# Kernel optimization log

Hardware: AMD Instinct MI355X
Metric: run time of the kernel (lower is better)

The kernel has to match this reference:

```python
import jax, jax.numpy as jnp
import numpy as np

N_EMBD = 2048
N_HEAD = 16
N_KV_HEAD = 4
HEAD_DIM = N_EMBD // N_HEAD
MAX_SEQ_LEN = 2048
EPS = 1e-6
ROPE_THETA = 10000.0


def _build_rope_cache(dim, max_seq_len, theta=ROPE_THETA):
    inv_freq = 1.0 / theta ** (np.arange(0, dim, 2, dtype=np.float32) / dim)
    t = np.arange(max_seq_len, dtype=np.float32)
    freqs = np.outer(t, inv_freq)
    emb = np.concatenate([freqs, freqs], axis=-1)
    return jnp.asarray(np.cos(emb)), jnp.asarray(np.sin(emb))


def _rotate_half(x):
    x1, x2 = jnp.split(x, 2, axis=-1)
    return jnp.concatenate([-x2, x1], axis=-1)


def _rms_norm(x, w, eps=EPS):
    var = jnp.mean(jnp.square(x), axis=-1, keepdims=True)
    return x * jax.lax.rsqrt(var + eps) * w


def setup_inputs() -> dict:
    key = jax.random.key(0)
    ks = jax.random.split(key, 7)
    s = 1.0 / np.sqrt(N_EMBD)
    kv_dim = N_KV_HEAD * HEAD_DIM
    x = jax.random.normal(ks[0], (2, 2048, N_EMBD), dtype=jnp.float32)
    Wq = jax.random.normal(ks[1], (N_EMBD, N_EMBD), dtype=jnp.float32) * s
    Wk = jax.random.normal(ks[2], (kv_dim, N_EMBD), dtype=jnp.float32) * s
    Wv = jax.random.normal(ks[3], (kv_dim, N_EMBD), dtype=jnp.float32) * s
    Wo = jax.random.normal(ks[4], (N_EMBD, N_EMBD), dtype=jnp.float32) * s
    qn_w = jnp.ones((HEAD_DIM,), dtype=jnp.float32)
    kn_w = jnp.ones((HEAD_DIM,), dtype=jnp.float32)
    cos, sin = _build_rope_cache(HEAD_DIM, MAX_SEQ_LEN)
    return {"x": x, "Wq": Wq, "Wk": Wk, "Wv": Wv, "Wo": Wo,
            "qn_w": qn_w, "kn_w": kn_w, "rope_cos": cos, "rope_sin": sin}


def reference(x, Wq, Wk, Wv, Wo, qn_w, kn_w, rope_cos, rope_sin):
    B, T, C = x.shape
    # projections (torch Linear: y = x @ W.T)
    q = jnp.einsum('btc,dc->btd', x, Wq).reshape(B, T, N_HEAD, HEAD_DIM).transpose(0, 2, 1, 3)
    k = jnp.einsum('btc,dc->btd', x, Wk).reshape(B, T, N_KV_HEAD, HEAD_DIM).transpose(0, 2, 1, 3)
    v = jnp.einsum('btc,dc->btd', x, Wv).reshape(B, T, N_KV_HEAD, HEAD_DIM).transpose(0, 2, 1, 3)
    # qk rms-norm
    q = _rms_norm(q, qn_w)
    k = _rms_norm(k, kn_w)
    # rope
    cos = rope_cos[:T][None, None]  # [1,1,T,D]
    sin = rope_sin[:T][None, None]
    q = q * cos + _rotate_half(q) * sin
    k = k * cos + _rotate_half(k) * sin
    # GQA broadcast: group queries over kv heads instead of repeating k/v
    G = N_HEAD // N_KV_HEAD
    qg = q.reshape(B, N_KV_HEAD, G, T, HEAD_DIM)
    scale = 1.0 / jnp.sqrt(jnp.asarray(HEAD_DIM, dtype=q.dtype))
    scores = jnp.einsum('bhgqd,bhkd->bhgqk', qg, k) * scale  # [B,KV,G,T,T]
    causal = jnp.tril(jnp.ones((T, T), dtype=bool))
    scores = jnp.where(causal, scores, jnp.asarray(-jnp.inf, dtype=scores.dtype))
    attn = jax.nn.softmax(scores, axis=-1)
    y = jnp.einsum('bhgqk,bhkd->bhgqd', attn, v)  # [B,KV,G,T,D]
    y = y.reshape(B, N_HEAD, T, HEAD_DIM).transpose(0, 2, 1, 3).reshape(B, T, C)
    return jnp.einsum('btc,dc->btd', y, Wo)
```

## Files before the change

kernel.cpp:

```cpp
#include <hip/hip_runtime.h>
#include <stdint.h>

typedef unsigned short u16;
typedef __attribute__((ext_vector_type(4))) float f32x4;
typedef __attribute__((ext_vector_type(16))) float f32x16;
typedef __attribute__((ext_vector_type(8))) short bf16x8;
typedef __attribute__((ext_vector_type(4))) unsigned short u16x4;
typedef __attribute__((ext_vector_type(4))) unsigned u32x4;

static __device__ __forceinline__ u16 f2bf(float f) {
  union { float f; unsigned u; } v; v.f = f;
  unsigned r = v.u + 0x7fffu + ((v.u >> 16) & 1u);
  return (u16)(r >> 16);
}

static __device__ __forceinline__ unsigned cvtpk(float lo, float hi) {
  unsigned r;
  asm("v_cvt_pk_bf16_f32 %0, %1, %2" : "=v"(r) : "v"(lo), "v"(hi));
  return r;
}

static __device__ __forceinline__ void plane32_swap(unsigned& a, unsigned& b) {
  asm volatile("v_permlane32_swap_b32 %0, %1" : "+v"(a), "+v"(b));
}

static __device__ __forceinline__ float exp2_fast(float x) {
  float r;
  asm("v_exp_f32 %0, %1" : "=v"(r) : "v"(x));
  return r;
}

static __device__ __forceinline__ void load_lds16(const void* g, void* l) {
  __builtin_amdgcn_global_load_lds(
      (const __attribute__((address_space(1))) void*)g,
      (__attribute__((address_space(3))) void*)l, 16, 0, 0);
}


__global__ __launch_bounds__(256) void cvt_f32_bf16(
    const float* __restrict__ in, u16* __restrict__ out, int n) {
  int i = blockIdx.x * 256 + threadIdx.x;
  const int n4 = n >> 2;
  for (; i < n4; i += gridDim.x * 256) {
    f32x4 v = *(const f32x4*)(in + (size_t)i * 4);
    u16x4 o = { f2bf(v[0]), f2bf(v[1]), f2bf(v[2]), f2bf(v[3]) };
    *(u16x4*)(out + (size_t)i * 4) = o;
  }
}

__global__ __launch_bounds__(256) void build_wcat(
    const float* __restrict__ Wq, const float* __restrict__ Wk,
    const float* __restrict__ Wv, u16* __restrict__ out) {
  int i = blockIdx.x * 256 + threadIdx.x;
  const int n4 = 3072 * 512;
  for (; i < n4; i += gridDim.x * 256) {
    int row = i >> 9;
    int c4 = i & 511;
    const float* src;
    if (row < 2048)       src = Wq + (size_t)row * 2048;
    else if (row < 2560)  src = Wk + (size_t)(row - 2048) * 2048;
    else                  src = Wv + (size_t)(row - 2560) * 2048;
    f32x4 v = *(const f32x4*)(src + c4 * 4);
    u16x4 o = { f2bf(v[0]), f2bf(v[1]), f2bf(v[2]), f2bf(v[3]) };
    *(u16x4*)(out + (size_t)i * 4) = o;
  }
}

__global__ __launch_bounds__(256) void gemm_bt(
    const u16* __restrict__ A, const u16* __restrict__ B,
    float* __restrict__ C, int M, int N, int K) {
  __shared__ u16 As[128 * 32];
  __shared__ u16 Bs[128 * 32];
  const int tid = threadIdx.x;
  const int lin = blockIdx.x;
  const int x = lin & 7, t = lin >> 3;
  const int bm = x * 4 + (t & 3);
  const int bn = t >> 2;
  const int w = tid >> 6, l = tid & 63;
  const int wr = w >> 1, wc = w & 1;
  const int lr = l & 15, lg = l >> 4;
  f32x4 acc[4][4] = {};
  const int srow = tid >> 2;
  const int scol = (tid & 3) << 3;
  const u16* Ag = A + (size_t)bm * 128 * K + (size_t)srow * K + scol;
  const u16* Bg = B + (size_t)bn * 128 * K + (size_t)srow * K + scol;
  u16* Asl = As + srow * 32 + scol;
  u16* Bsl = Bs + srow * 32 + scol;
  const int nk = K >> 5;
  for (int kt = 0; kt < nk; ++kt) {
    __syncthreads();
    const int ko = kt << 5;
    load_lds16(Ag + ko, Asl);
    load_lds16(Ag + (size_t)64 * K + ko, Asl + 64 * 32);
    load_lds16(Bg + ko, Bsl);
    load_lds16(Bg + (size_t)64 * K + ko, Bsl + 64 * 32);
    __syncthreads();
    bf16x8 af[4], bfr[4];
#pragma unroll
    for (int m = 0; m < 4; ++m)
      af[m] = *(const bf16x8*)&As[(wr * 64 + m * 16 + lr) * 32 + lg * 8];
#pragma unroll
    for (int n = 0; n < 4; ++n)
      bfr[n] = *(const bf16x8*)&Bs[(wc * 64 + n * 16 + lr) * 32 + lg * 8];
#pragma unroll
    for (int m = 0; m < 4; ++m)
#pragma unroll
      for (int n = 0; n < 4; ++n)
        acc[m][n] = __builtin_amdgcn_mfma_f32_16x16x32_bf16(af[m], bfr[n], acc[m][n], 0, 0, 0);
  }
#pragma unroll
  for (int m = 0; m < 4; ++m) {
    const int row = bm * 128 + wr * 64 + m * 16 + lg * 4;
#pragma unroll
    for (int n = 0; n < 4; ++n) {
      const int col = bn * 128 + wc * 64 + n * 16 + lr;
#pragma unroll
      for (int r = 0; r < 4; ++r)
        C[(size_t)(row + r) * N + col] = acc[m][n][r];
    }
  }
}

__global__ __launch_bounds__(256) void norm_rope(
    const float* __restrict__ qkv, const float* __restrict__ qn_w,
    const float* __restrict__ kn_w, const float* __restrict__ cosb,
    const float* __restrict__ sinb, u16* __restrict__ qhat,
    u16* __restrict__ khat) {
  const int gw = (blockIdx.x * 256 + threadIdx.x) >> 6;
  const int lane = threadIdx.x & 63;
  const int slot = gw % 20;
  const int row = gw / 20;
  const int t = row & 2047;
  const int b = row >> 11;
  const float* src; const float* nw; u16* dst;
  bool isq = slot < 16;
  if (isq) {
    src = qkv + (size_t)row * 3072 + slot * 128;
    nw = qn_w;
    dst = qhat + ((size_t)(b * 16 + slot) * 2048 + t) * 128;
  } else {
    src = qkv + (size_t)row * 3072 + 2048 + (slot - 16) * 128;
    nw = kn_w;
    dst = khat + ((size_t)(b * 4 + (slot - 16)) * 2048 + t) * 128;
  }
  float x1 = src[lane], x2 = src[lane + 64];
  float ss = x1 * x1 + x2 * x2;
#pragma unroll
  for (int o = 32; o; o >>= 1) ss += __shfl_xor(ss, o);
  float rs = rsqrtf(ss * (1.0f / 128.0f) + 1e-6f);
  float h1 = x1 * rs * nw[lane];
  float h2 = x2 * rs * nw[lane + 64];
  float c = cosb[t * 128 + lane], s = sinb[t * 128 + lane];
  float o1 = h1 * c - h2 * s;
  float o2 = h2 * c + h1 * s;
  if (isq) { o1 *= 0.12751744752f; o2 *= 0.12751744752f; }
  dst[lane] = f2bf(o1);
  dst[lane + 64] = f2bf(o2);
}

__global__ __launch_bounds__(256) void v_trans(
    const float* __restrict__ qkv, u16* __restrict__ vT) {
  __shared__ u16 st[64][130];
  const int bi = blockIdx.x;
  const int tt = bi & 31;
  const int kv = (bi >> 5) & 3;
  const int b = bi >> 7;
  const int tid = threadIdx.x;
#pragma unroll
  for (int i = 0; i < 32; ++i) {
    int idx = i * 256 + tid;
    int t = idx >> 7, d = idx & 127;
    float v = qkv[(size_t)(b * 2048 + tt * 64 + t) * 3072 + 2560 + kv * 128 + d];
    st[t][d] = f2bf(v);
  }
  __syncthreads();
#pragma unroll
  for (int i = 0; i < 32; ++i) {
    int idx = i * 256 + tid;
    int d = idx >> 6, t = idx & 63;
    vT[((size_t)(b * 4 + kv) * 128 + d) * 2048 + tt * 64 + t] = st[t][d];
  }
}

__global__ __launch_bounds__(512, 2) void attn(
    const u16* __restrict__ qhat, const u16* __restrict__ khat,
    const u16* __restrict__ vT, u16* __restrict__ yb) {
  __shared__ u16 Kt[2][64 * 128];
  __shared__ u16 Vt[2][128 * 64];
  const int bi = blockIdx.x;
  const int s = bi & 7;
  const int bh = bi >> 3;
  const int h = bh & 15, b = bh >> 4;
  const int kvh = h >> 2;
  const int tid = threadIdx.x;
  const int w = tid >> 6, l = tid & 63;
  const int ws = w & 3;
  const int cw = (w < 4) ? s : (15 - s);
  const int ql = l & 31, hi = l >> 5;
  const int wq0 = cw * 128 + ws * 32;
  const int wq_end = wq0 + 31;
  const int qg = wq0 + ql;

  bf16x8 qf[8];
  const u16* qp = qhat + ((size_t)(b * 16 + h) * 2048 + qg) * 128 + hi * 8;
#pragma unroll
  for (int sf = 0; sf < 8; ++sf) qf[sf] = *(const bf16x8*)(qp + 16 * sf);

  f32x16 yacc[4] = {};
  float m = -1e30f, lsum = 0.f;

  const u16* Kg = khat + (size_t)(b * 4 + kvh) * 2048 * 128;
  const u16* Vg = vT + (size_t)(b * 4 + kvh) * 128 * 2048;
  const int nt = 32 - 2 * s;

  auto stageK = [&](int tile, int buf) {
#pragma unroll
    for (int j = 0; j < 2; ++j) {
      int idx = j * 512 + tid;
      int row = idx >> 4, ch = idx & 15;
      load_lds16(Kg + (size_t)(tile * 64 + row) * 128 + ((ch ^ (row & 7)) * 8),
                 &Kt[buf][idx * 8]);
    }
  };
  auto stageV = [&](int tile, int buf) {
#pragma unroll
    for (int j = 0; j < 2; ++j) {
      int idx = j * 512 + tid;
      int row = idx >> 3, ch = idx & 7;
      load_lds16(Vg + (size_t)row * 2048 + tile * 64 + ((ch ^ (row & 7)) * 8),
                 &Vt[buf][idx * 8]);
    }
  };

  stageK(0, 0);
  stageV(0, 0);
  int cur = 0;
  for (int tile = 0; tile < nt; ++tile) {
    const int kv0 = tile * 64;
    __syncthreads();
    if (tile + 1 < nt) { stageK(tile + 1, cur ^ 1); stageV(tile + 1, cur ^ 1); }
    if (kv0 <= wq_end) {
      const u16* Kc = Kt[cur];
      const u16* Vc = Vt[cur];
      f32x16 sacc[2] = {};
      __builtin_amdgcn_s_setprio(1);
#pragma unroll
      for (int n = 0; n < 2; ++n) {
#pragma unroll
        for (int sf = 0; sf < 8; ++sf) {
          bf16x8 kf = *(const bf16x8*)&Kc[(n * 32 + ql) * 128 + (((2 * sf + hi) ^ (l & 7)) * 8)];
          sacc[n] = __builtin_amdgcn_mfma_f32_32x32x16_bf16(kf, qf[sf], sacc[n], 0, 0, 0);
        }
      }
      __builtin_amdgcn_s_setprio(0);
      if (kv0 + 63 > wq0) {
#pragma unroll
        for (int n = 0; n < 2; ++n)
#pragma unroll
          for (int r = 0; r < 16; ++r) {
            int kv = kv0 + n * 32 + (r & 3) + 8 * (r >> 2) + 4 * hi;
            if (kv > qg) sacc[n][r] = -1e30f;
          }
      }
      float pm = -1e30f;
#pragma unroll
      for (int n = 0; n < 2; ++n)
#pragma unroll
        for (int r = 0; r < 16; ++r) pm = fmaxf(pm, sacc[n][r]);
      pm = fmaxf(pm, __shfl_xor(pm, 32));
      if (!__all(pm - m <= 11.0f)) {
        float mn = fmaxf(m, pm);
        float sc = exp2_fast(m - mn);
        m = mn;
        lsum *= sc;
#pragma unroll
        for (int r = 0; r < 16; ++r) {
          int row = (r & 3) + 8 * (r >> 2) + 4 * hi;
          float scr = __shfl(sc, row);
#pragma unroll
          for (int d = 0; d < 4; ++d) yacc[d][r] *= scr;
        }
      }
      float ls = 0.f;
#pragma unroll
      for (int n = 0; n < 2; ++n)
#pragma unroll
        for (int r = 0; r < 16; ++r) {
          float e = exp2_fast(sacc[n][r] - m);
          sacc[n][r] = e;
          ls += e;
        }
      ls += __shfl_xor(ls, 32);
      lsum += ls;
      bf16x8 pa[4];
#pragma unroll
      for (int s4 = 0; s4 < 4; ++s4) {
        const int n = s4 >> 1, R = (s4 & 1) * 8;
        unsigned P01 = cvtpk(sacc[n][R + 0], sacc[n][R + 1]);
        unsigned P23 = cvtpk(sacc[n][R + 2], sacc[n][R + 3]);
        unsigned P45 = cvtpk(sacc[n][R + 4], sacc[n][R + 5]);
        unsigned P67 = cvtpk(sacc[n][R + 6], sacc[n][R + 7]);
        plane32_swap(P01, P45);
        plane32_swap(P23, P67);
        union { u32x4 u; bf16x8 bv; } cvu;
        cvu.u[0] = P01; cvu.u[1] = P23; cvu.u[2] = P45; cvu.u[3] = P67;
        pa[s4] = cvu.bv;
      }
      __builtin_amdgcn_s_setprio(1);
#pragma unroll
      for (int d = 0; d < 4; ++d) {
        const int rv = d * 32 + ql;
#pragma unroll
        for (int ks = 0; ks < 4; ++ks) {
          bf16x8 vf = *(const bf16x8*)&Vc[rv * 64 + (((ks * 2 + hi) ^ (rv & 7)) * 8)];
          yacc[d] = __builtin_amdgcn_mfma_f32_32x32x16_bf16(pa[ks], vf, yacc[d], 0, 0, 0);
        }
      }
      __builtin_amdgcn_s_setprio(0);
    }
    cur ^= 1;
  }
#pragma unroll
  for (int r = 0; r < 16; ++r) {
    int row = (r & 3) + 8 * (r >> 2) + 4 * hi;
    float li = __shfl(lsum, row);
    float inv = 1.0f / li;
    u16* yp = yb + ((size_t)(b * 2048) + wq0 + row) * 2048 + h * 128 + ql;
#pragma unroll
    for (int d = 0; d < 4; ++d) yp[d * 32] = f2bf(yacc[d][r] * inv);
  }
}


extern "C" void kernel_launch(void* const* d_in, const int* in_sizes, int n_in,
                              void* d_out, int out_size, void* d_ws, size_t ws_size,
                              hipStream_t stream) {
  const float* x    = (const float*)d_in[0];
  const float* Wq   = (const float*)d_in[1];
  const float* Wk   = (const float*)d_in[2];
  const float* Wv   = (const float*)d_in[3];
  const float* Wo   = (const float*)d_in[4];
  const float* qn   = (const float*)d_in[5];
  const float* kn   = (const float*)d_in[6];
  const float* cosb = (const float*)d_in[7];
  const float* sinb = (const float*)d_in[8];
  float* out = (float*)d_out;
  (void)in_sizes; (void)n_in; (void)out_size; (void)ws_size;

  char* p = (char*)d_ws;
  u16*   xb   = (u16*)p;   p += (size_t)8388608 * 2;
  u16*   wcat = (u16*)p;   p += (size_t)6291456 * 2;
  u16*   wob  = (u16*)p;   p += (size_t)4194304 * 2;
  float* qkvf = (float*)p; p += (size_t)12582912 * 4;
  u16*   qh   = (u16*)p;   p += (size_t)8388608 * 2;
  u16*   kh   = (u16*)p;   p += (size_t)2097152 * 2;
  u16*   vt   = (u16*)p;   p += (size_t)2097152 * 2;
  u16*   yb   = (u16*)p;   p += (size_t)8388608 * 2;

  cvt_f32_bf16<<<2048, 256, 0, stream>>>(x, xb, 8388608);
  build_wcat<<<2048, 256, 0, stream>>>(Wq, Wk, Wv, wcat);
  cvt_f32_bf16<<<2048, 256, 0, stream>>>(Wo, wob, 4194304);
  gemm_bt<<<768, 256, 0, stream>>>(xb, wcat, qkvf, 4096, 3072, 2048);
  norm_rope<<<20480, 256, 0, stream>>>(qkvf, qn, kn, cosb, sinb, qh, kh);
  v_trans<<<256, 256, 0, stream>>>(qkvf, vt);
  attn<<<256, 512, 0, stream>>>(qh, kh, vt, yb);
  gemm_bt<<<512, 256, 0, stream>>>(yb, wob, out, 4096, 2048, 2048);
}
```

Baseline: 242.1 us.

## Switch GEMM to 32x32x16 MFMA with XOR-swizzled LDS layout

Replaces the 16x16x32 bf16 MFMA tiling in gemm_bt with 32x32x16 MFMA tiles, using 2x2 f32x16 accumulators per wave. The global-to-LDS load now XOR-swizzles the 16-byte column chunk by row, so fragment reads from LDS avoid bank conflicts. This is meant to cut the number of LDS fragment loads and MFMA issues per K tile. The output write pattern changes to the 32x32 accumulator layout, and that store stays uncoalesced.

```diff
diff --git a/kernel.cpp b/kernel.cpp
--- a/kernel.cpp
+++ b/kernel.cpp
@@ -78,14 +78,14 @@
   const int bn = t >> 2;
   const int w = tid >> 6, l = tid & 63;
   const int wr = w >> 1, wc = w & 1;
-  const int lr = l & 15, lg = l >> 4;
-  f32x4 acc[4][4] = {};
+  const int ql = l & 31, hi = l >> 5;
+  f32x16 acc[2][2] = {};
   const int srow = tid >> 2;
-  const int scol = (tid & 3) << 3;
+  const int scol = (((tid & 3) ^ (srow & 3)) << 3);
   const u16* Ag = A + (size_t)bm * 128 * K + (size_t)srow * K + scol;
   const u16* Bg = B + (size_t)bn * 128 * K + (size_t)srow * K + scol;
-  u16* Asl = As + srow * 32 + scol;
-  u16* Bsl = Bs + srow * 32 + scol;
+  u16* Asl = As + tid * 8;
+  u16* Bsl = Bs + tid * 8;
   const int nk = K >> 5;
   for (int kt = 0; kt < nk; ++kt) {
     __syncthreads();
@@ -95,28 +95,36 @@
     load_lds16(Bg + ko, Bsl);
     load_lds16(Bg + (size_t)64 * K + ko, Bsl + 64 * 32);
     __syncthreads();
-    bf16x8 af[4], bfr[4];
-#pragma unroll
-    for (int m = 0; m < 4; ++m)
-      af[m] = *(const bf16x8*)&As[(wr * 64 + m * 16 + lr) * 32 + lg * 8];
-#pragma unroll
-    for (int n = 0; n < 4; ++n)
-      bfr[n] = *(const bf16x8*)&Bs[(wc * 64 + n * 16 + lr) * 32 + lg * 8];
-#pragma unroll
-    for (int m = 0; m < 4; ++m)
-#pragma unroll
-      for (int n = 0; n < 4; ++n)
-        acc[m][n] = __builtin_amdgcn_mfma_f32_16x16x32_bf16(af[m], bfr[n], acc[m][n], 0, 0, 0);
-  }
-#pragma unroll
-  for (int m = 0; m < 4; ++m) {
-    const int row = bm * 128 + wr * 64 + m * 16 + lg * 4;
-#pragma unroll
-    for (int n = 0; n < 4; ++n) {
-      const int col = bn * 128 + wc * 64 + n * 16 + lr;
-#pragma unroll
-      for (int r = 0; r < 4; ++r)
-        C[(size_t)(row + r) * N + col] = acc[m][n][r];
+#pragma unroll
+    for (int ks = 0; ks < 2; ++ks) {
+      const int e = ks * 2 + hi;
+      bf16x8 af[2], bfr[2];
+#pragma unroll
+      for (int ti = 0; ti < 2; ++ti) {
+        const int ra = wr * 64 + ti * 32 + ql;
+        const int rb = wc * 64 + ti * 32 + ql;
+        af[ti]  = *(const bf16x8*)&As[ra * 32 + ((e ^ (ra & 3)) << 3)];
+        bfr[ti] = *(const bf16x8*)&Bs[rb * 32 + ((e ^ (rb & 3)) << 3)];
+      }
+#pragma unroll
+      for (int mi = 0; mi < 2; ++mi)
+#pragma unroll
+        for (int ni = 0; ni < 2; ++ni)
+          acc[mi][ni] = __builtin_amdgcn_mfma_f32_32x32x16_bf16(
+              af[mi], bfr[ni], acc[mi][ni], 0, 0, 0);
+    }
+  }
+#pragma unroll
+  for (int mi = 0; mi < 2; ++mi) {
+    const int rb0 = bm * 128 + wr * 64 + mi * 32;
+#pragma unroll
+    for (int ni = 0; ni < 2; ++ni) {
+      const int col = bn * 128 + wc * 64 + ni * 32 + ql;
+#pragma unroll
+      for (int r = 0; r < 16; ++r) {
+        const int row = rb0 + (r & 3) + 8 * (r >> 2) + 4 * hi;
+        C[(size_t)row * N + col] = acc[mi][ni][r];
+      }
     }
   }
 }
```

New measurement: 238.2 us. No clear change (-1.6%).

## Rework GEMM to 32x32 MFMA with 64-deep swizzled LDS tiles and bf16 QKV output

Applied to the files above, without the earlier changes.

The GEMM core now uses 32x32x16 bf16 MFMA tiles with a K-step of 64, and the LDS layout is XOR-swizzled to avoid bank conflicts. This halves the number of barrier iterations and raises the math done per LDS read. The QKV projection now writes bf16 instead of fp32, which halves the intermediate traffic for norm_rope and v_trans. The cost is extra rounding of q/k before the RMS norm, and double the LDS per block.

```diff
diff --git a/kernel.cpp b/kernel.cpp
--- a/kernel.cpp
+++ b/kernel.cpp
@@ -12,6 +12,10 @@
   union { float f; unsigned u; } v; v.f = f;
   unsigned r = v.u + 0x7fffu + ((v.u >> 16) & 1u);
   return (u16)(r >> 16);
+}
+static __device__ __forceinline__ float bf2f(u16 u) {
+  union { unsigned u; float f; } v; v.u = ((unsigned)u) << 16;
+  return v.f;
 }
 
 static __device__ __forceinline__ unsigned cvtpk(float lo, float hi) {
@@ -66,63 +70,78 @@
   }
 }
 
+#define GEMM_CORE(C_STORE)                                                            \
+  __shared__ u16 As[128 * 64];                                                        \
+  __shared__ u16 Bs[128 * 64];                                                        \
+  const int tid = threadIdx.x;                                                        \
+  const int lin = blockIdx.x;                                                         \
+  const int x = lin & 7, t = lin >> 3;                              \
+  const int bm = x * 4 + (t & 3);                                                     \
+  const int bn = t >> 2;                                                              \
+  const int w = tid >> 6, l = tid & 63;                                               \
+  const int wr = w >> 1, wc = w & 1;                                                  \
+  const int ql = l & 31, hi = l >> 5;                                                 \
+  f32x16 acc[2][2] = {};                                                              \
+  const int nk = K >> 6;                                                              \
+  for (int kt = 0; kt < nk; ++kt) {                                                   \
+    __syncthreads();                                                                  \
+    const int ko = kt << 6;                                                           \
+    _Pragma("unroll")                                                                 \
+    for (int j = 0; j < 4; ++j) {                                                     \
+      int idx = j * 256 + tid;                                                        \
+      int row = idx >> 3, ch = idx & 7;                                               \
+      int col = ko + (((ch ^ (row & 7))) << 3);                                       \
+      load_lds16(A + (size_t)(bm * 128 + row) * K + col, As + idx * 8);               \
+      load_lds16(B + (size_t)(bn * 128 + row) * K + col, Bs + idx * 8);               \
+    }                                                                                 \
+    __syncthreads();                                                                  \
+    _Pragma("unroll")                                                                 \
+    for (int ks = 0; ks < 4; ++ks) {                                                  \
+      const int e = ks * 2 + hi;                                                      \
+      bf16x8 af[2], bfr[2];                                                           \
+      _Pragma("unroll")                                                               \
+      for (int ti = 0; ti < 2; ++ti) {                                                \
+        const int ra = wr * 64 + ti * 32 + ql;                                        \
+        const int rb = wc * 64 + ti * 32 + ql;                                        \
+        af[ti]  = *(const bf16x8*)&As[ra * 64 + ((e ^ (ra & 7)) << 3)];               \
+        bfr[ti] = *(const bf16x8*)&Bs[rb * 64 + ((e ^ (rb & 7)) << 3)];               \
+      }                                                                               \
+      _Pragma("unroll")                                                               \
+      for (int mi = 0; mi < 2; ++mi)                                                  \
+        _Pragma("unroll")                                                             \
+        for (int ni = 0; ni < 2; ++ni)                                                \
+          acc[mi][ni] = __builtin_amdgcn_mfma_f32_32x32x16_bf16(                      \
+              af[mi], bfr[ni], acc[mi][ni], 0, 0, 0);                                 \
+    }                                                                                 \
+  }                                                                                   \
+  _Pragma("unroll")                                                                   \
+  for (int mi = 0; mi < 2; ++mi) {                                                    \
+    const int rb0 = bm * 128 + wr * 64 + mi * 32;                                     \
+    _Pragma("unroll")                                                                 \
+    for (int ni = 0; ni < 2; ++ni) {                                                  \
+      const int col = bn * 128 + wc * 64 + ni * 32 + ql;                              \
+      _Pragma("unroll")                                                               \
+      for (int r = 0; r < 16; ++r) {                                                  \
+        const int row = rb0 + (r & 3) + 8 * (r >> 2) + 4 * hi;                        \
+        C_STORE;                                                                      \
+      }                                                                               \
+    }                                                                                 \
+  }
+
+__global__ __launch_bounds__(256) void gemm_bt16(
+    const u16* __restrict__ A, const u16* __restrict__ B,
+    u16* __restrict__ C, int M, int N, int K) {
+  GEMM_CORE(C[(size_t)row * N + col] = f2bf(acc[mi][ni][r]))
+}
+
 __global__ __launch_bounds__(256) void gemm_bt(
     const u16* __restrict__ A, const u16* __restrict__ B,
     float* __restrict__ C, int M, int N, int K) {
-  __shared__ u16 As[128 * 32];
-  __shared__ u16 Bs[128 * 32];
-  const int tid = threadIdx.x;
-  const int lin = blockIdx.x;
-  const int x = lin & 7, t = lin >> 3;
-  const int bm = x * 4 + (t & 3);
-  const int bn = t >> 2;
-  const int w = tid >> 6, l = tid & 63;
-  const int wr = w >> 1, wc = w & 1;
-  const int lr = l & 15, lg = l >> 4;
-  f32x4 acc[4][4] = {};
-  const int srow = tid >> 2;
-  const int scol = (tid & 3) << 3;
-  const u16* Ag = A + (size_t)bm * 128 * K + (size_t)srow * K + scol;
-  const u16* Bg = B + (size_t)bn * 128 * K + (size_t)srow * K + scol;
-  u16* Asl = As + srow * 32 + scol;
-  u16* Bsl = Bs + srow * 32 + scol;
-  const int nk = K >> 5;
-  for (int kt = 0; kt < nk; ++kt) {
-    __syncthreads();
-    const int ko = kt << 5;
-    load_lds16(Ag + ko, Asl);
-    load_lds16(Ag + (size_t)64 * K + ko, Asl + 64 * 32);
-    load_lds16(Bg + ko, Bsl);
-    load_lds16(Bg + (size_t)64 * K + ko, Bsl + 64 * 32);
-    __syncthreads();
-    bf16x8 af[4], bfr[4];
-#pragma unroll
-    for (int m = 0; m < 4; ++m)
-      af[m] = *(const bf16x8*)&As[(wr * 64 + m * 16 + lr) * 32 + lg * 8];
-#pragma unroll
-    for (int n = 0; n < 4; ++n)
-      bfr[n] = *(const bf16x8*)&Bs[(wc * 64 + n * 16 + lr) * 32 + lg * 8];
-#pragma unroll
-    for (int m = 0; m < 4; ++m)
-#pragma unroll
-      for (int n = 0; n < 4; ++n)
-        acc[m][n] = __builtin_amdgcn_mfma_f32_16x16x32_bf16(af[m], bfr[n], acc[m][n], 0, 0, 0);
-  }
-#pragma unroll
-  for (int m = 0; m < 4; ++m) {
-    const int row = bm * 128 + wr * 64 + m * 16 + lg * 4;
-#pragma unroll
-    for (int n = 0; n < 4; ++n) {
-      const int col = bn * 128 + wc * 64 + n * 16 + lr;
-#pragma unroll
-      for (int r = 0; r < 4; ++r)
-        C[(size_t)(row + r) * N + col] = acc[m][n][r];
-    }
-  }
+  GEMM_CORE(C[(size_t)row * N + col] = acc[mi][ni][r])
 }
 
 __global__ __launch_bounds__(256) void norm_rope(
-    const float* __restrict__ qkv, const float* __restrict__ qn_w,
+    const u16* __restrict__ qkv, const float* __restrict__ qn_w,
     const float* __restrict__ kn_w, const float* __restrict__ cosb,
     const float* __restrict__ sinb, u16* __restrict__ qhat,
     u16* __restrict__ khat) {
@@ -132,7 +151,7 @@
   const int row = gw / 20;
   const int t = row & 2047;
   const int b = row >> 11;
-  const float* src; const float* nw; u16* dst;
+  const u16* src; const float* nw; u16* dst;
   bool isq = slot < 16;
   if (isq) {
     src = qkv + (size_t)row * 3072 + slot * 128;
@@ -143,7 +162,7 @@
     nw = kn_w;
     dst = khat + ((size_t)(b * 4 + (slot - 16)) * 2048 + t) * 128;
   }
-  float x1 = src[lane], x2 = src[lane + 64];
+  float x1 = bf2f(src[lane]), x2 = bf2f(src[lane + 64]);
   float ss = x1 * x1 + x2 * x2;
 #pragma unroll
   for (int o = 32; o; o >>= 1) ss += __shfl_xor(ss, o);
@@ -159,7 +178,7 @@
 }
 
 __global__ __launch_bounds__(256) void v_trans(
-    const float* __restrict__ qkv, u16* __restrict__ vT) {
+    const u16* __restrict__ qkv, u16* __restrict__ vT) {
   __shared__ u16 st[64][130];
   const int bi = blockIdx.x;
   const int tt = bi & 31;
@@ -170,8 +189,7 @@
   for (int i = 0; i < 32; ++i) {
     int idx = i * 256 + tid;
     int t = idx >> 7, d = idx & 127;
-    float v = qkv[(size_t)(b * 2048 + tt * 64 + t) * 3072 + 2560 + kv * 128 + d];
-    st[t][d] = f2bf(v);
+    st[t][d] = qkv[(size_t)(b * 2048 + tt * 64 + t) * 3072 + 2560 + kv * 128 + d];
   }
   __syncthreads();
 #pragma unroll
@@ -351,7 +369,7 @@
   u16*   xb   = (u16*)p;   p += (size_t)8388608 * 2;
   u16*   wcat = (u16*)p;   p += (size_t)6291456 * 2;
   u16*   wob  = (u16*)p;   p += (size_t)4194304 * 2;
-  float* qkvf = (float*)p; p += (size_t)12582912 * 4;
+  u16*   qkvb = (u16*)p;   p += (size_t)12582912 * 2;
   u16*   qh   = (u16*)p;   p += (size_t)8388608 * 2;
   u16*   kh   = (u16*)p;   p += (size_t)2097152 * 2;
   u16*   vt   = (u16*)p;   p += (size_t)2097152 * 2;
@@ -360,9 +378,9 @@
   cvt_f32_bf16<<<2048, 256, 0, stream>>>(x, xb, 8388608);
   build_wcat<<<2048, 256, 0, stream>>>(Wq, Wk, Wv, wcat);
   cvt_f32_bf16<<<2048, 256, 0, stream>>>(Wo, wob, 4194304);
-  gemm_bt<<<768, 256, 0, stream>>>(xb, wcat, qkvf, 4096, 3072, 2048);
-  norm_rope<<<20480, 256, 0, stream>>>(qkvf, qn, kn, cosb, sinb, qh, kh);
-  v_trans<<<256, 256, 0, stream>>>(qkvf, vt);
+  gemm_bt16<<<768, 256, 0, stream>>>(xb, wcat, qkvb, 4096, 3072, 2048);
+  norm_rope<<<20480, 256, 0, stream>>>(qkvb, qn, kn, cosb, sinb, qh, kh);
+  v_trans<<<256, 256, 0, stream>>>(qkvb, vt);
   attn<<<256, 512, 0, stream>>>(qh, kh, vt, yb);
   gemm_bt<<<512, 256, 0, stream>>>(yb, wob, out, 4096, 2048, 2048);
 }
```

After: 215.4 us. -11.0%, faster.
